# Optimization experiments

Hardware: AMD Instinct MI355X
Metric: run time of the kernel (lower is better)

The kernel has to match this reference:

```python
import jax, jax.numpy as jnp
import numpy as np

T = 35        # points per voxel
D, H, W = 10, 400, 352  # voxel grid (KITTI car setting)
EPS = 1e-5    # BatchNorm eps


def setup_inputs() -> dict:
    key = jax.random.key(0)
    ks = jax.random.split(key, 10)
    K = 15000  # non-empty voxels in the frame
    feature = jax.random.normal(ks[0], (K, T, 7), jnp.float32)
    # realistic padding: each voxel has 5..35 valid points, rest zero
    npts = jax.random.randint(ks[1], (K,), 5, T + 1)
    valid = jnp.arange(T)[None, :] < npts[:, None]
    feature = feature * valid[:, :, None].astype(jnp.float32)
    c_b = jnp.zeros((K, 1), jnp.int32)
    c_d = jax.random.randint(ks[2], (K, 1), 0, D).astype(jnp.int32)
    c_h = jax.random.randint(ks[3], (K, 1), 0, H).astype(jnp.int32)
    c_w = jax.random.randint(ks[4], (K, 1), 0, W).astype(jnp.int32)
    coordinate = jnp.concatenate([c_b, c_d, c_h, c_w], axis=1)
    W1 = jax.random.normal(ks[5], (7, 16), jnp.float32) * 0.1
    b1 = jnp.zeros((16,), jnp.float32)
    g1 = jnp.ones((16,), jnp.float32)
    be1 = jnp.zeros((16,), jnp.float32)
    W2 = jax.random.normal(ks[6], (32, 64), jnp.float32) * 0.1
    b2 = jnp.zeros((64,), jnp.float32)
    g2 = jnp.ones((64,), jnp.float32)
    be2 = jnp.zeros((64,), jnp.float32)
    return {"feature": feature, "coordinate": coordinate, "bs": 1,
            "W1": W1, "b1": b1, "g1": g1, "be1": be1,
            "W2": W2, "b2": b2, "g2": g2, "be2": be2}


def _vfe(x, mask, Wm, b, g, be):
    # Linear + ReLU per point: [K, T, cin] -> [K, T, cmid]
    pw = jax.nn.relu(jnp.einsum('ktc,cd->ktd', x, Wm) + b)
    # BatchNorm1d (training mode): per-channel stats over (K, T), biased var
    mu = pw.mean(axis=(0, 1))
    var = pw.var(axis=(0, 1))
    pw = (pw - mu) * jax.lax.rsqrt(var + EPS) * g + be
    # max over points, broadcast-concat (VoxelNet VFE)
    agg = pw.max(axis=1, keepdims=True)               # [K, 1, cmid]
    cat = jnp.concatenate([pw, jnp.broadcast_to(agg, pw.shape)], axis=-1)
    return cat * mask  # mask padded points


def reference(feature, coordinate, bs, W1, b1, g1, be1, W2, b2, g2, be2):
    # mask: point is valid if its channel-wise max != 0 (as in original)
    vmax = feature.max(axis=2, keepdims=True)          # [K, T, 1]
    mask = (vmax != 0).astype(feature.dtype)
    x = _vfe(feature, mask, W1, b1, g1, be1)           # [K, T, 32]
    x = _vfe(x, mask, W2, b2, g2, be2)                 # [K, T, 128]
    voxelwise = x.max(axis=1)                          # [K, 128]
    # scatter into dense grid (sparse COO -> to_dense sums duplicates)
    out = jnp.zeros((bs, D, H, W, 128), feature.dtype)
    out = out.at[coordinate[:, 0], coordinate[:, 1],
                 coordinate[:, 2], coordinate[:, 3]].add(voxelwise)
    return out
```

## Files before the change

### kernel.cpp

```cpp
#include <hip/hip_runtime.h>
#include <math.h>

#define KVOX 15000
#define TP 35
#define CIN 7
#define CM1 16
#define CM2 64
#define NPTS (KVOX * TP)
#define DD 10
#define HH 400
#define WWID 352
#define NCELL (DD * HH * WWID)
#define EPSBN 1e-5f
#define NB1 256
#define NBV 3750

typedef float vfloat4 __attribute__((ext_vector_type(4)));
typedef int   vint4   __attribute__((ext_vector_type(4)));

#define NT4 (NCELL / 4)
#define NC4 (KVOX * 128 / 4)
#define NBI ((NT4 + NC4 + 255) / 256)
__global__ __launch_bounds__(256) void init_kernel(vint4* __restrict__ table4,
                                                   vfloat4* __restrict__ comp4)
{
    int i = blockIdx.x * 256 + threadIdx.x;
    if (i < NT4) {
        table4[i] = (vint4){0x7FFFFFFF, 0x7FFFFFFF, 0x7FFFFFFF, 0x7FFFFFFF};
    } else if (i - NT4 < NC4) {
        comp4[i - NT4] = (vfloat4){0.f, 0.f, 0.f, 0.f};
    }
}

__global__ __launch_bounds__(256) void stats1_kernel(
    const float* __restrict__ feat, const int* __restrict__ coord,
    const float* __restrict__ W1, const float* __restrict__ b1,
    float* __restrict__ partial1, int* __restrict__ table)
{
    __shared__ float w1s[CIN * CM1];
    __shared__ float b1s[CM1];
    __shared__ float red[4][32];
    int tid = threadIdx.x;
    if (tid < CIN * CM1) w1s[tid] = W1[tid];
    if (tid < CM1) b1s[tid] = b1[tid];

    int g = blockIdx.x * 256 + tid;
    if (g < KVOX) {
        int cell = (coord[g * 4 + 1] * HH + coord[g * 4 + 2]) * WWID + coord[g * 4 + 3];
        atomicMin(&table[cell], g);
    }
    __syncthreads();

    float s[CM1], q[CM1];
#pragma unroll
    for (int c = 0; c < CM1; ++c) { s[c] = 0.f; q[c] = 0.f; }

    for (int i = blockIdx.x * 256 + tid; i < NPTS; i += NB1 * 256) {
        float f[CIN];
#pragma unroll
        for (int j = 0; j < CIN; ++j) f[j] = feat[(size_t)i * CIN + j];
#pragma unroll
        for (int c = 0; c < CM1; ++c) {
            float acc = b1s[c];
#pragma unroll
            for (int j = 0; j < CIN; ++j) acc = fmaf(f[j], w1s[j * CM1 + c], acc);
            float pw = fmaxf(acc, 0.f);
            s[c] += pw; q[c] += pw * pw;
        }
    }
#pragma unroll
    for (int c = 0; c < CM1; ++c) {
#pragma unroll
        for (int off = 32; off > 0; off >>= 1) {
            s[c] += __shfl_xor(s[c], off);
            q[c] += __shfl_xor(q[c], off);
        }
    }
    int wid = tid >> 6, lane = tid & 63;
    if (lane == 0) {
#pragma unroll
        for (int c = 0; c < CM1; ++c) { red[wid][c] = s[c]; red[wid][CM1 + c] = q[c]; }
    }
    __syncthreads();
    if (tid < 32)
        partial1[blockIdx.x * 32 + tid] =
            red[0][tid] + red[1][tid] + red[2][tid] + red[3][tid];
}

__global__ __launch_bounds__(256) void reduce1_kernel(
    const float* __restrict__ partial1, const float* __restrict__ g1,
    const float* __restrict__ be1, float* __restrict__ coef1)
{
    __shared__ float acc[8][32];
    __shared__ float tot[32];
    int tid = threadIdx.x;
    int c = tid & 31, part = tid >> 5;
    float v = 0.f;
    for (int b = part; b < NB1; b += 8) v += partial1[b * 32 + c];
    acc[part][c] = v;
    __syncthreads();
    if (tid < 32) {
        float t = 0.f;
#pragma unroll
        for (int p = 0; p < 8; ++p) t += acc[p][tid];
        tot[tid] = t;
    }
    __syncthreads();
    if (tid < CM1) {
        float inv = 1.f / (float)NPTS;
        float mu = tot[tid] * inv;
        float var = tot[CM1 + tid] * inv - mu * mu;
        float a = g1[tid] * rsqrtf(var + EPSBN);
        coef1[tid] = a;
        coef1[CM1 + tid] = be1[tid] - mu * a;
    }
}

template <bool FINAL>
__global__ __launch_bounds__(256) void vfe_kernel(
    const float* __restrict__ feat,
    const float* __restrict__ W1g, const float* __restrict__ b1g,
    const float* __restrict__ coef1,
    const float* __restrict__ W2g, const float* __restrict__ b2g,
    const float* __restrict__ coef2,
    const int*  __restrict__ coord,
    const int*  __restrict__ table,
    float* __restrict__ partial2,
    float* __restrict__ compact)
{
    __shared__ float sfeat[4][TP * CIN + 11];
    alignas(16) __shared__ float scat[4][TP * 32];
    __shared__ float smask[4][TP + 5];
    __shared__ float red2[4][2 * CM2];

    int tid = threadIdx.x, wid = tid >> 6, lane = tid & 63;
    int k = blockIdx.x * 4 + wid;
    int tg = lane >> 4, c1 = lane & 15;

    float w1r[CIN];
#pragma unroll
    for (int j = 0; j < CIN; ++j) w1r[j] = W1g[j * CM1 + c1];
    float b1r = b1g[c1];
    float a1r = coef1[c1], d1r = coef1[CM1 + c1];
    float w2r[32];
#pragma unroll
    for (int j = 0; j < 32; ++j) w2r[j] = W2g[j * CM2 + lane];
    float b2r = b2g[lane];
    float a2r = 0.f, d2r = 0.f;
    if constexpr (FINAL) { a2r = coef2[lane]; d2r = coef2[CM2 + lane]; }

    float* F = sfeat[wid];
    float* CT = scat[wid];
    float* M = smask[wid];

    for (int i = lane; i < TP * CIN; i += 64)
        F[i] = feat[(size_t)k * (TP * CIN) + i];
    __syncthreads();

    float maxv = -INFINITY;
#pragma unroll
    for (int it = 0; it < 9; ++it) {
        int t = tg + 4 * it;
        if (t < TP) {
            float fv0 = F[t * CIN];
            float m7 = fv0;
            float acc = fmaf(fv0, w1r[0], b1r);
#pragma unroll
            for (int j = 1; j < CIN; ++j) {
                float fv = F[t * CIN + j];
                m7 = fmaxf(m7, fv);
                acc = fmaf(fv, w1r[j], acc);
            }
            float maskv = (m7 != 0.f) ? 1.f : 0.f;
            float pw = fmaxf(acc, 0.f);
            float bn = fmaf(pw, a1r, d1r);
            maxv = fmaxf(maxv, bn);
            CT[t * 32 + c1] = bn * maskv;
            if (c1 == 0) M[t] = maskv;
        }
    }
    maxv = fmaxf(maxv, __shfl_xor(maxv, 16));
    maxv = fmaxf(maxv, __shfl_xor(maxv, 32));
#pragma unroll
    for (int it = 0; it < 9; ++it) {
        int t = tg + 4 * it;
        if (t < TP) CT[t * 32 + 16 + c1] = maxv * M[t];
    }

    float s_acc = 0.f, q_acc = 0.f;
    float agg2 = -INFINITY, v1 = -INFINITY, mmin = 1.f;
    for (int t = 0; t < TP; ++t) {
        const float4* r4 = reinterpret_cast<const float4*>(&CT[t * 32]);
        float acc0 = b2r, acc1 = 0.f;
#pragma unroll
        for (int i = 0; i < 8; i += 2) {
            float4 va = r4[i], vb = r4[i + 1];
            acc0 = fmaf(va.x, w2r[4 * i + 0], acc0);
            acc0 = fmaf(va.y, w2r[4 * i + 1], acc0);
            acc0 = fmaf(va.z, w2r[4 * i + 2], acc0);
            acc0 = fmaf(va.w, w2r[4 * i + 3], acc0);
            acc1 = fmaf(vb.x, w2r[4 * i + 4], acc1);
            acc1 = fmaf(vb.y, w2r[4 * i + 5], acc1);
            acc1 = fmaf(vb.z, w2r[4 * i + 6], acc1);
            acc1 = fmaf(vb.w, w2r[4 * i + 7], acc1);
        }
        float pw = fmaxf(acc0 + acc1, 0.f);
        if constexpr (!FINAL) {
            s_acc += pw; q_acc += pw * pw;
        } else {
            float bn = fmaf(pw, a2r, d2r);
            agg2 = fmaxf(agg2, bn);
            float mk = M[t];
            v1 = fmaxf(v1, bn * mk);
            mmin = fminf(mmin, mk);
        }
    }

    if constexpr (!FINAL) {
        red2[wid][lane] = s_acc;
        red2[wid][CM2 + lane] = q_acc;
        __syncthreads();
        if (tid < 2 * CM2)
            partial2[(size_t)blockIdx.x * (2 * CM2) + tid] =
                red2[0][tid] + red2[1][tid] + red2[2][tid] + red2[3][tid];
    } else {
        float v2 = (mmin == 0.f) ? fmaxf(agg2, 0.f) : agg2;
        int cell = (coord[k * 4 + 1] * HH + coord[k * 4 + 2]) * WWID + coord[k * 4 + 3];
        int w = table[cell];
        atomicAdd(&compact[(size_t)w * 128 + lane], v1);
        atomicAdd(&compact[(size_t)w * 128 + 64 + lane], v2);
    }
}

__global__ __launch_bounds__(256) void reduce2_kernel(
    const float* __restrict__ partial2, const float* __restrict__ g2,
    const float* __restrict__ be2, float* __restrict__ coef2)
{
    __shared__ float sred[4][2];
    int c = blockIdx.x;
    int tid = threadIdx.x;
    float s = 0.f, q = 0.f;
    for (int r = tid; r < NBV; r += 256) {
        s += partial2[(size_t)r * 128 + c];
        q += partial2[(size_t)r * 128 + CM2 + c];
    }
#pragma unroll
    for (int off = 32; off > 0; off >>= 1) {
        s += __shfl_xor(s, off);
        q += __shfl_xor(q, off);
    }
    int wid = tid >> 6;
    if ((tid & 63) == 0) { sred[wid][0] = s; sred[wid][1] = q; }
    __syncthreads();
    if (tid == 0) {
        float S = sred[0][0] + sred[1][0] + sred[2][0] + sred[3][0];
        float Q = sred[0][1] + sred[1][1] + sred[2][1] + sred[3][1];
        float inv = 1.f / (float)NPTS;
        float mu = S * inv;
        float var = Q * inv - mu * mu;
        float a = g2[c] * rsqrtf(var + EPSBN);
        coef2[c] = a;
        coef2[CM2 + c] = be2[c] - mu * a;
    }
}

#define NWT (NCELL * 32 / 4)
#define NBW (NWT / 256)
__global__ __launch_bounds__(256) void write_kernel(
    vfloat4* __restrict__ out, const int* __restrict__ table,
    const float* __restrict__ compact)
{
    int t = blockIdx.x * 256 + threadIdx.x;
    size_t f4 = (size_t)t * 4;
    int cell = (int)(f4 >> 5);
    int w = table[cell];
    if (w < KVOX) {
        const vfloat4* src =
            reinterpret_cast<const vfloat4*>(&compact[(size_t)w * 128 + ((f4 & 31) << 2)]);
        out[f4 + 0] = src[0]; out[f4 + 1] = src[1];
        out[f4 + 2] = src[2]; out[f4 + 3] = src[3];
    } else {
        const vfloat4 z = {0.f, 0.f, 0.f, 0.f};
        out[f4 + 0] = z; out[f4 + 1] = z; out[f4 + 2] = z; out[f4 + 3] = z;
    }
}

extern "C" void kernel_launch(void* const* d_in, const int* in_sizes, int n_in,
                              void* d_out, int out_size, void* d_ws, size_t ws_size,
                              hipStream_t stream)
{
    const float* feat = (const float*)d_in[0];
    const int*   coord = (const int*)d_in[1];
    const float* W1  = (const float*)d_in[3];
    const float* b1  = (const float*)d_in[4];
    const float* g1  = (const float*)d_in[5];
    const float* be1 = (const float*)d_in[6];
    const float* W2  = (const float*)d_in[7];
    const float* b2  = (const float*)d_in[8];
    const float* g2  = (const float*)d_in[9];
    const float* be2 = (const float*)d_in[10];
    float* out = (float*)d_out;

    int*   table    = (int*)d_ws;
    float* compact  = (float*)d_ws + NCELL;
    float* partial1 = compact + KVOX * 128;
    float* partial2 = partial1 + NB1 * 32;
    float* coef1    = partial2 + NBV * 128;
    float* coef2    = coef1 + 32;

    init_kernel<<<NBI, 256, 0, stream>>>((vint4*)table, (vfloat4*)compact);
    stats1_kernel<<<NB1, 256, 0, stream>>>(feat, coord, W1, b1, partial1, table);
    reduce1_kernel<<<1, 256, 0, stream>>>(partial1, g1, be1, coef1);
    vfe_kernel<false><<<NBV, 256, 0, stream>>>(feat, W1, b1, coef1, W2, b2,
                                               nullptr, nullptr, nullptr,
                                               partial2, nullptr);
    reduce2_kernel<<<CM2, 256, 0, stream>>>(partial2, g2, be2, coef2);
    vfe_kernel<true><<<NBV, 256, 0, stream>>>(feat, W1, b1, coef1, W2, b2,
                                              coef2, coord, table,
                                              nullptr, compact);
    write_kernel<<<NBW, 256, 0, stream>>>((vfloat4*)out, table, compact);
}
```

Before: 935.7 us.

## Compute layer-2 VFE once, storing per-voxel pre-BN max/min extrema

Removes the second full VFE pass by saving, per voxel and channel, the max and min of the pre-BatchNorm activations (over masked and over all points) during the statistics pass. A small finalize kernel then applies the affine BN and picks max or min depending on the sign of the scale, which holds because an affine map is monotonic. Zeroing the compact buffer moves into the VFE kernel, and the write kernel now issues one float4 per thread. The trade is an extra 15 MB extents buffer plus one more launch.

```diff
diff --git a/kernel.cpp b/kernel.cpp
--- a/kernel.cpp
+++ b/kernel.cpp
@@ -19,17 +19,10 @@
 typedef int   vint4   __attribute__((ext_vector_type(4)));
 
 #define NT4 (NCELL / 4)
-#define NC4 (KVOX * 128 / 4)
-#define NBI ((NT4 + NC4 + 255) / 256)
-__global__ __launch_bounds__(256) void init_kernel(vint4* __restrict__ table4,
-                                                   vfloat4* __restrict__ comp4)
+__global__ __launch_bounds__(256) void init_kernel(vint4* __restrict__ table4)
 {
     int i = blockIdx.x * 256 + threadIdx.x;
-    if (i < NT4) {
-        table4[i] = (vint4){0x7FFFFFFF, 0x7FFFFFFF, 0x7FFFFFFF, 0x7FFFFFFF};
-    } else if (i - NT4 < NC4) {
-        comp4[i - NT4] = (vfloat4){0.f, 0.f, 0.f, 0.f};
-    }
+    table4[i] = (vint4){0x7FFFFFFF, 0x7FFFFFFF, 0x7FFFFFFF, 0x7FFFFFFF};
 }
 
 __global__ __launch_bounds__(256) void stats1_kernel(
@@ -116,17 +109,15 @@
     }
 }
 
-template <bool FINAL>
-__global__ __launch_bounds__(256) void vfe_kernel(
+__global__ __launch_bounds__(256) void vfe_once_kernel(
     const float* __restrict__ feat,
     const float* __restrict__ W1g, const float* __restrict__ b1g,
     const float* __restrict__ coef1,
     const float* __restrict__ W2g, const float* __restrict__ b2g,
-    const float* __restrict__ coef2,
-    const int*  __restrict__ coord,
-    const int*  __restrict__ table,
     float* __restrict__ partial2,
-    float* __restrict__ compact)
+    float* __restrict__ ext,
+    int*   __restrict__ flags,
+    vfloat4* __restrict__ compact4)
 {
     __shared__ float sfeat[4][TP * CIN + 11];
     alignas(16) __shared__ float scat[4][TP * 32];
@@ -146,8 +137,6 @@
 #pragma unroll
     for (int j = 0; j < 32; ++j) w2r[j] = W2g[j * CM2 + lane];
     float b2r = b2g[lane];
-    float a2r = 0.f, d2r = 0.f;
-    if constexpr (FINAL) { a2r = coef2[lane]; d2r = coef2[CM2 + lane]; }
 
     float* F = sfeat[wid];
     float* CT = scat[wid];
@@ -188,7 +177,9 @@
     }
 
     float s_acc = 0.f, q_acc = 0.f;
-    float agg2 = -INFINITY, v1 = -INFINITY, mmin = 1.f;
+    float pwmax_v = -INFINITY, pwmin_v = INFINITY;
+    float pwmax_a = -INFINITY, pwmin_a = INFINITY;
+    float mmin = 1.f;
     for (int t = 0; t < TP; ++t) {
         const float4* r4 = reinterpret_cast<const float4*>(&CT[t * 32]);
         float acc0 = b2r, acc1 = 0.f;
@@ -205,31 +196,29 @@
             acc1 = fmaf(vb.w, w2r[4 * i + 7], acc1);
         }
         float pw = fmaxf(acc0 + acc1, 0.f);
-        if constexpr (!FINAL) {
-            s_acc += pw; q_acc += pw * pw;
-        } else {
-            float bn = fmaf(pw, a2r, d2r);
-            agg2 = fmaxf(agg2, bn);
-            float mk = M[t];
-            v1 = fmaxf(v1, bn * mk);
-            mmin = fminf(mmin, mk);
-        }
-    }
-
-    if constexpr (!FINAL) {
-        red2[wid][lane] = s_acc;
-        red2[wid][CM2 + lane] = q_acc;
-        __syncthreads();
-        if (tid < 2 * CM2)
-            partial2[(size_t)blockIdx.x * (2 * CM2) + tid] =
-                red2[0][tid] + red2[1][tid] + red2[2][tid] + red2[3][tid];
-    } else {
-        float v2 = (mmin == 0.f) ? fmaxf(agg2, 0.f) : agg2;
-        int cell = (coord[k * 4 + 1] * HH + coord[k * 4 + 2]) * WWID + coord[k * 4 + 3];
-        int w = table[cell];
-        atomicAdd(&compact[(size_t)w * 128 + lane], v1);
-        atomicAdd(&compact[(size_t)w * 128 + 64 + lane], v2);
-    }
+        s_acc += pw; q_acc += pw * pw;
+        float mk = M[t];
+        mmin = fminf(mmin, mk);
+        pwmax_a = fmaxf(pwmax_a, pw);
+        pwmin_a = fminf(pwmin_a, pw);
+        pwmax_v = fmaxf(pwmax_v, (mk != 0.f) ? pw : -INFINITY);
+        pwmin_v = fminf(pwmin_v, (mk != 0.f) ? pw : INFINITY);
+    }
+
+    float* E = ext + (size_t)k * 256;
+    E[lane] = pwmax_v; E[64 + lane] = pwmin_v;
+    E[128 + lane] = pwmax_a; E[192 + lane] = pwmin_a;
+    if (lane == 0) flags[k] = (mmin == 0.f) ? 1 : 0;
+
+    red2[wid][lane] = s_acc;
+    red2[wid][CM2 + lane] = q_acc;
+    __syncthreads();
+    if (tid < 2 * CM2)
+        partial2[(size_t)blockIdx.x * (2 * CM2) + tid] =
+            red2[0][tid] + red2[1][tid] + red2[2][tid] + red2[3][tid];
+
+    if (tid < 128)
+        compact4[(size_t)blockIdx.x * 128 + tid] = (vfloat4){0.f, 0.f, 0.f, 0.f};
 }
 
 __global__ __launch_bounds__(256) void reduce2_kernel(
@@ -264,25 +253,36 @@
     }
 }
 
-#define NWT (NCELL * 32 / 4)
-#define NBW (NWT / 256)
+__global__ __launch_bounds__(256) void finalize_kernel(
+    const float* __restrict__ ext, const int* __restrict__ flags,
+    const int* __restrict__ coord, const float* __restrict__ coef2,
+    const int* __restrict__ table, float* __restrict__ compact)
+{
+    int tid = threadIdx.x;
+    int k = blockIdx.x * 2 + (tid >> 7);
+    int sub = tid & 127;
+    int c = sub & 63, half = sub >> 6;
+    float a = coef2[c], d = coef2[CM2 + c];
+    const float* E = ext + (size_t)k * 256 + half * 128;
+    float hi = E[c], lo = E[64 + c];
+    float val = (a >= 0.f) ? fmaf(a, hi, d) : fmaf(a, lo, d);
+    if (flags[k]) val = fmaxf(val, 0.f);
+    int cell = (coord[k * 4 + 1] * HH + coord[k * 4 + 2]) * WWID + coord[k * 4 + 3];
+    int w = table[cell];
+    atomicAdd(&compact[(size_t)w * 128 + sub], val);
+}
+
+#define NBW (NCELL * 32 / 256)
 __global__ __launch_bounds__(256) void write_kernel(
     vfloat4* __restrict__ out, const int* __restrict__ table,
-    const float* __restrict__ compact)
-{
-    int t = blockIdx.x * 256 + threadIdx.x;
-    size_t f4 = (size_t)t * 4;
-    int cell = (int)(f4 >> 5);
+    const vfloat4* __restrict__ compact4)
+{
+    int i = blockIdx.x * 256 + threadIdx.x;
+    int cell = i >> 5;
     int w = table[cell];
-    if (w < KVOX) {
-        const vfloat4* src =
-            reinterpret_cast<const vfloat4*>(&compact[(size_t)w * 128 + ((f4 & 31) << 2)]);
-        out[f4 + 0] = src[0]; out[f4 + 1] = src[1];
-        out[f4 + 2] = src[2]; out[f4 + 3] = src[3];
-    } else {
-        const vfloat4 z = {0.f, 0.f, 0.f, 0.f};
-        out[f4 + 0] = z; out[f4 + 1] = z; out[f4 + 2] = z; out[f4 + 3] = z;
-    }
+    vfloat4 v = {0.f, 0.f, 0.f, 0.f};
+    if (w < KVOX) v = compact4[w * 32 + (i & 31)];
+    out[i] = v;
 }
 
 extern "C" void kernel_launch(void* const* d_in, const int* in_sizes, int n_in,
@@ -303,20 +303,21 @@
 
     int*   table    = (int*)d_ws;
     float* compact  = (float*)d_ws + NCELL;
-    float* partial1 = compact + KVOX * 128;
+    float* ext      = compact + (size_t)KVOX * 128;
+    float* partial1 = ext + (size_t)KVOX * 256;
     float* partial2 = partial1 + NB1 * 32;
-    float* coef1    = partial2 + NBV * 128;
+    int*   flags    = (int*)(partial2 + NBV * 128);
+    float* coef1    = (float*)(flags + KVOX);
     float* coef2    = coef1 + 32;
 
-    init_kernel<<<NBI, 256, 0, stream>>>((vint4*)table, (vfloat4*)compact);
+    init_kernel<<<NT4 / 256, 256, 0, stream>>>((vint4*)table);
     stats1_kernel<<<NB1, 256, 0, stream>>>(feat, coord, W1, b1, partial1, table);
     reduce1_kernel<<<1, 256, 0, stream>>>(partial1, g1, be1, coef1);
-    vfe_kernel<false><<<NBV, 256, 0, stream>>>(feat, W1, b1, coef1, W2, b2,
-                                               nullptr, nullptr, nullptr,
-                                               partial2, nullptr);
+    vfe_once_kernel<<<NBV, 256, 0, stream>>>(feat, W1, b1, coef1, W2, b2,
+                                             partial2, ext, flags,
+                                             (vfloat4*)compact);
     reduce2_kernel<<<CM2, 256, 0, stream>>>(partial2, g2, be2, coef2);
-    vfe_kernel<true><<<NBV, 256, 0, stream>>>(feat, W1, b1, coef1, W2, b2,
-                                              coef2, coord, table,
-                                              nullptr, compact);
-    write_kernel<<<NBW, 256, 0, stream>>>((vfloat4*)out, table, compact);
-}
+    finalize_kernel<<<KVOX / 2, 256, 0, stream>>>(ext, flags, coord, coef2,
+                                                  table, compact);
+    write_kernel<<<NBW, 256, 0, stream>>>((vfloat4*)out, table, (vfloat4*)compact);
+}
```

After: 836.4 us. -10.6%, faster.
